# Performance work log

Measured on AMD Instinct MI355X. Metric: run time of the kernel, lower is better.

Reference implementation:

```python
import jax, jax.numpy as jnp
import numpy as np

N, E, ESM, H, OUT, L, NG = 20000, 640000, 1280, 128, 256, 3, 64
NV, EV = 4, 1  # node/edge vector channels
MSG_S, MSG_V = 2 * H + H, 2 * NV + EV   # 384, 9
UPD_S, UPD_V = 2 * H, 2 * NV            # 256, 8


def _safe_norm(v):
    # exact ||v|| with zero (not nan) gradient at v == 0
    n2 = jnp.sum(v * v, axis=-1)
    pos = n2 > 0
    return jnp.sqrt(jnp.where(pos, n2, 1.0)) * pos


def _normalize(x, eps=1e-12):
    n = _safe_norm(x)[..., None]
    return jnp.where(n > 0, x / jnp.maximum(n, eps), 0.0)


def _ln(x, g, b, eps=1e-5):
    m = x.mean(-1, keepdims=True)
    v = ((x - m) ** 2).mean(-1, keepdims=True)
    return (x - m) / jnp.sqrt(v + eps) * g + b


def _gvp(s, v, Wss, Wvs, Wsv, Wvv, g, b):
    # s: [M, Cs], v: [M, Cv, 3]
    vn = _safe_norm(v)                                        # [M, Cv]
    s_out = jax.nn.gelu(_ln(s @ Wss.T + vn @ Wvs.T, g, b), approximate=False)
    v_out = jnp.einsum('mic,oi->moc', v, Wvv)                 # [M, Cvo, 3]
    v_out = v_out * jax.nn.sigmoid(s @ Wsv.T)[:, :, None]     # gate from input s
    return s_out, v_out


def _compute_node_vectors(coords, cb):
    ca_cb = _normalize(cb - coords)
    ca_next = jnp.roll(coords, -1, axis=0)
    d = (ca_next - coords).at[-1].set(0.0)
    d = _normalize(d)
    normal = _normalize(jnp.cross(ca_cb, d))
    t = (ca_next - jnp.roll(coords, 1, axis=0)).at[0].set(0.0).at[-1].set(0.0)
    t = _normalize(t)
    return jnp.stack([ca_cb, d, normal, t], axis=1)           # [N, 4, 3]


def setup_inputs() -> dict:
    key = jax.random.key(0)
    ks = jax.random.split(key, 32)

    def w(k, shape):
        return (jax.random.normal(k, shape, jnp.float32) / np.sqrt(shape[-1])).astype(jnp.float32)

    inp = {
        'esm_features': jax.random.normal(ks[0], (N, ESM), jnp.float32),
        'geometric_features': jax.random.normal(ks[1], (N, 15), jnp.float32),
        'node_coords': jax.random.normal(ks[2], (N, 3), jnp.float32) * 10.0,
        'edge_index': jax.random.randint(ks[3], (2, E), 0, N, jnp.int32),
        'edge_attr': jax.random.normal(ks[4], (E, 16), jnp.float32),
        'batch_index': jnp.sort(jax.random.randint(ks[5], (N,), 0, NG, jnp.int32)),
        # projections
        'node_proj_W': w(ks[6], (H, ESM + 9)), 'node_proj_b': jnp.zeros((H,), jnp.float32),
        'edge_proj_W': w(ks[7], (H, 13)), 'edge_proj_b': jnp.zeros((H,), jnp.float32),
        # message GVP (stacked over L layers)
        'msg_Wss': w(ks[8], (L, H, MSG_S)), 'msg_Wvs': w(ks[9], (L, H, MSG_V)),
        'msg_Wsv': w(ks[10], (L, NV, MSG_S)), 'msg_Wvv': w(ks[11], (L, NV, MSG_V)),
        'msg_ln_g': jnp.ones((L, H), jnp.float32), 'msg_ln_b': jnp.zeros((L, H), jnp.float32),
        # update GVP
        'upd_Wss': w(ks[12], (L, H, UPD_S)), 'upd_Wvs': w(ks[13], (L, H, UPD_V)),
        'upd_Wsv': w(ks[14], (L, NV, UPD_S)), 'upd_Wvv': w(ks[15], (L, NV, UPD_V)),
        'upd_ln_g': jnp.ones((L, H), jnp.float32), 'upd_ln_b': jnp.zeros((L, H), jnp.float32),
        # heads
        'node_out_W': w(ks[16], (ESM, H)), 'node_out_b': jnp.zeros((ESM,), jnp.float32),
        'graph_out_W': w(ks[17], (OUT, H)), 'graph_out_b': jnp.zeros((OUT,), jnp.float32),
    }
    return inp


def reference(esm_features, geometric_features, node_coords, edge_index, edge_attr,
              batch_index, node_proj_W, node_proj_b, edge_proj_W, edge_proj_b,
              msg_Wss, msg_Wvs, msg_Wsv, msg_Wvv, msg_ln_g, msg_ln_b,
              upd_Wss, upd_Wvs, upd_Wsv, upd_Wvv, upd_ln_g, upd_ln_b,
              node_out_W, node_out_b, graph_out_W, graph_out_b):
    n = esm_features.shape[0]
    cb = geometric_features[:, 3:6]
    geo_scalar = geometric_features[:, 6:15]
    node_s = jnp.concatenate([esm_features, geo_scalar], -1) @ node_proj_W.T + node_proj_b
    node_v = _compute_node_vectors(node_coords, cb)
    edge_s = jnp.concatenate([edge_attr[:, 0:2], edge_attr[:, 5:]], -1) @ edge_proj_W.T + edge_proj_b
    edge_v = edge_attr[:, 2:5][:, None, :]                    # [E, 1, 3]
    src, dst = edge_index[0], edge_index[1]
    for l in range(msg_Wss.shape[0]):
        ms = jnp.concatenate([node_s[src], node_s[dst], edge_s], -1)   # [E, 3H]
        mv = jnp.concatenate([node_v[src], node_v[dst], edge_v], 1)    # [E, 9, 3]
        ms, mv = _gvp(ms, mv, msg_Wss[l], msg_Wvs[l], msg_Wsv[l], msg_Wvv[l],
                      msg_ln_g[l], msg_ln_b[l])
        ag_s = jnp.zeros((n, ms.shape[1]), ms.dtype).at[dst].add(ms)
        ag_v = jnp.zeros((n, mv.shape[1], 3), mv.dtype).at[dst].add(mv)
        us = jnp.concatenate([node_s, ag_s], -1)
        uv = jnp.concatenate([node_v, ag_v], 1)
        ns, nv = _gvp(us, uv, upd_Wss[l], upd_Wvs[l], upd_Wsv[l], upd_Wvv[l],
                      upd_ln_g[l], upd_ln_b[l])
        node_s = node_s + ns
        node_v = node_v + nv
    updated_nodes = node_s @ node_out_W.T + node_out_b
    gfeat = node_s @ graph_out_W.T + graph_out_b
    cnt = jax.ops.segment_sum(jnp.ones((n,), gfeat.dtype), batch_index, NG)
    graph_emb = jax.ops.segment_sum(gfeat, batch_index, NG) / jnp.maximum(cnt, 1.0)[:, None]
    return graph_emb, updated_nodes
```

## Files before the change

kernel.cpp:

```cpp
#include <hip/hip_runtime.h>
#include <math.h>

#define DEVI __device__ __forceinline__

namespace {

constexpr int NN = 20000;
constexpr int NE = 640000;

typedef __attribute__((ext_vector_type(8))) short s8v;
typedef __attribute__((ext_vector_type(4))) float f4v;

DEVI float gelu_f(float x){ return 0.5f*x*(1.0f+erff(x*0.70710678118654752440f)); }
DEVI float gelu_t(float x){
  float u = x*x;
  float z = x*(1.59576912f + 0.07135481f*u);
  return x / (1.f + __expf(-z));
}
DEVI float sigm(float x){ return 1.0f/(1.0f+expf(-x)); }
DEVI float sigm_f(float x){ return 1.0f/(1.0f+__expf(-x)); }
DEVI unsigned bf_rne(float f){ unsigned u=__float_as_uint(f); return (u + 0x7fffu + ((u>>16)&1u)) >> 16; }

struct F3{ float x,y,z; };
DEVI F3 sub3(F3 a, F3 b){ return F3{a.x-b.x, a.y-b.y, a.z-b.z}; }
DEVI F3 cross3(F3 a, F3 b){ return F3{a.y*b.z-a.z*b.y, a.z*b.x-a.x*b.z, a.x*b.y-a.y*b.x}; }
DEVI F3 snorm3(F3 v){
  float n2 = v.x*v.x+v.y*v.y+v.z*v.z;
  if(n2 > 0.f){ float inv = 1.0f/sqrtf(n2); return F3{v.x*inv, v.y*inv, v.z*inv}; }
  return F3{0.f,0.f,0.f};
}

__global__ void k_prep(const float* __restrict__ npW, const float* __restrict__ noW,
                       const float* __restrict__ goW,
                       const float* __restrict__ mWss, const float* __restrict__ mWvs,
                       const float* __restrict__ uWss, const float* __restrict__ uWvs,
                       unsigned short* __restrict__ npW_bf, float* __restrict__ Wt_no,
                       float* __restrict__ Wt_go,
                       float* __restrict__ Wt_mss, float* __restrict__ Wt_mvs,
                       float* __restrict__ Wt_uss, float* __restrict__ Wt_uvs){
  int b = blockIdx.x, t = threadIdx.x;
  if(b >= 1563){
    int idx = (b-1563)*256 + t;
    if(idx < 128*1408){
      int r = idx/1408, c = idx-r*1408;
      npW_bf[idx] = (c<1289) ? (unsigned short)bf_rne(npW[(size_t)r*1289+c]) : (unsigned short)0;
    }
    return;
  }
  const float* src; float* dst; int R,C,ld,base,elems;
  if(b<640){ src=noW; dst=Wt_no; R=1280;C=128;ld=128; base=0; elems=163840; }
  else if(b<768){ src=goW; dst=Wt_go; R=256;C=128;ld=128; base=640; elems=32768; }
  else {
    int bb=b-768; int l=bb/265; int r=bb-l*265;
    if(r<128){ src=mWss+(size_t)l*128*384; dst=Wt_mss+(size_t)l*256*128; R=128;C=256;ld=384; base=768+l*265; elems=32768; }
    else if(r<133){ src=mWvs+(size_t)l*128*9; dst=Wt_mvs+(size_t)l*9*128; R=128;C=9;ld=9; base=768+l*265+128; elems=1152; }
    else if(r<261){ src=uWss+(size_t)l*128*256; dst=Wt_uss+(size_t)l*256*128; R=128;C=256;ld=256; base=768+l*265+133; elems=32768; }
    else { src=uWvs+(size_t)l*128*8; dst=Wt_uvs+(size_t)l*8*128; R=128;C=8;ld=8; base=768+l*265+261; elems=1024; }
  }
  int idx=(b-base)*256+t;
  if(idx>=elems) return;
  int r=idx/C, c=idx%C;
  dst[c*R+r] = src[r*ld+c];
}

__global__ void k_conv(const float* __restrict__ esm, const float* __restrict__ geo,
                       unsigned short* __restrict__ esm_bf){
  int idx = blockIdx.x*256 + threadIdx.x;
  if(idx >= 20000*176) return;
  int r = idx/176, c = idx - r*176;
  int k = c*8;
  float v0,v1,v2,v3,v4,v5,v6,v7;
  if(k+8 <= 1280){
    const float4* p = reinterpret_cast<const float4*>(esm + (size_t)r*1280 + k);
    float4 x=p[0], y=p[1];
    v0=x.x;v1=x.y;v2=x.z;v3=x.w;v4=y.x;v5=y.y;v6=y.z;v7=y.w;
  } else {
    float vv[8];
#pragma unroll
    for(int j=0;j<8;j++){
      int kk=k+j;
      vv[j] = (kk<1280)? esm[(size_t)r*1280+kk] : ((kk<1289)? geo[r*15+6+(kk-1280)] : 0.f);
    }
    v0=vv[0];v1=vv[1];v2=vv[2];v3=vv[3];v4=vv[4];v5=vv[5];v6=vv[6];v7=vv[7];
  }
  uint4 w;
  w.x = bf_rne(v0) | (bf_rne(v1)<<16);
  w.y = bf_rne(v2) | (bf_rne(v3)<<16);
  w.z = bf_rne(v4) | (bf_rne(v5)<<16);
  w.w = bf_rne(v6) | (bf_rne(v7)<<16);
  reinterpret_cast<uint4*>(esm_bf)[idx] = w;
}

__global__ __launch_bounds__(256,4) void k_init(
    const unsigned short* __restrict__ esm_bf, const unsigned short* __restrict__ npW_bf,
    float* __restrict__ part){
  int t = threadIdx.x;
  int b = blockIdx.x;
  int ks = b & 3, nb = b >> 2;
  int wv = t>>6, lane = t&63;
  int row0 = nb*64 + wv*16;
  int arow = row0 + (lane&15);
  int arc = (arow < NN) ? arow : (NN-1);
  int kb = (lane>>4)*8;
  const unsigned short* ap = esm_bf + (size_t)arc*1408 + ks*352 + kb;
  const unsigned short* bp = npW_bf + (size_t)(lane&15)*1408 + ks*352 + kb;
  f4v acc[8];
#pragma unroll
  for(int i=0;i<8;i++) acc[i] = (f4v){0.f,0.f,0.f,0.f};
  for(int c=0;c<11;c++){
    s8v a = *reinterpret_cast<const s8v*>(ap + c*32);
#pragma unroll
    for(int nt=0;nt<8;nt++){
      s8v bb = *reinterpret_cast<const s8v*>(bp + (size_t)nt*16*1408 + c*32);
      acc[nt] = __builtin_amdgcn_mfma_f32_16x16x32_bf16(a, bb, acc[nt], 0,0,0);
    }
  }
  float* po = part + (size_t)ks*NN*128;
  int col = lane&15, r4 = (lane>>4)*4;
#pragma unroll
  for(int nt=0;nt<8;nt++){
    int o = nt*16+col;
#pragma unroll
    for(int r=0;r<4;r++){
      int row = row0 + r4 + r;
      if(row<NN) po[(size_t)row*128+o] = acc[nt][r];
    }
  }
}

__global__ void k_reduce(const float* __restrict__ part, const float* __restrict__ bias,
                         float* __restrict__ node_s){
  int idx = blockIdx.x*256 + threadIdx.x;
  int o = idx & 127;
  node_s[idx] = bias[o] + part[idx] + part[(size_t)NN*128+idx]
              + part[2*(size_t)NN*128+idx] + part[3*(size_t)NN*128+idx];
}

__global__ void k_nodevec(const float* __restrict__ coords, const float* __restrict__ geo,
                          float* __restrict__ node_v,
                          int* __restrict__ counts, int* __restrict__ cntg){
  int n = blockIdx.x*256 + threadIdx.x;
  if(n<64) cntg[n]=0;
  if(n>=NN) return;
  counts[n]=0;
  F3 c  {coords[n*3], coords[n*3+1], coords[n*3+2]};
  F3 cb {geo[n*15+3], geo[n*15+4], geo[n*15+5]};
  F3 cacb = snorm3(sub3(cb, c));
  F3 d{0.f,0.f,0.f};
  if(n < NN-1){
    F3 nx {coords[(n+1)*3], coords[(n+1)*3+1], coords[(n+1)*3+2]};
    d = snorm3(sub3(nx, c));
  }
  F3 nor = snorm3(cross3(cacb, d));
  F3 tv{0.f,0.f,0.f};
  if(n>0 && n<NN-1){
    F3 nx {coords[(n+1)*3], coords[(n+1)*3+1], coords[(n+1)*3+2]};
    F3 pv {coords[(n-1)*3], coords[(n-1)*3+1], coords[(n-1)*3+2]};
    tv = snorm3(sub3(nx, pv));
  }
  float* p = node_v + n*12;
  p[0]=cacb.x; p[1]=cacb.y; p[2]=cacb.z;
  p[3]=d.x;    p[4]=d.y;    p[5]=d.z;
  p[6]=nor.x;  p[7]=nor.y;  p[8]=nor.z;
  p[9]=tv.x;   p[10]=tv.y;  p[11]=tv.z;
}

__global__ void k_hist(const int* __restrict__ eidx, const int* __restrict__ batch,
                       int* __restrict__ counts, int* __restrict__ cntg){
  int i = blockIdx.x*256+threadIdx.x;
  if(i<NE) atomicAdd(&counts[eidx[NE+i]], 1);
  if(i<NN) atomicAdd(&cntg[batch[i]], 1);
}
__global__ void k_scan1(const int* __restrict__ counts, int* __restrict__ bsums){
  __shared__ int red[256];
  int b=blockIdx.x, t=threadIdx.x;
  int base=b*512;
  int v=0;
  for(int i=t;i<512;i+=256){ int g=base+i; if(g<NN) v+=counts[g]; }
  red[t]=v; __syncthreads();
  for(int s=128;s;s>>=1){ if(t<s) red[t]+=red[t+s]; __syncthreads(); }
  if(t==0) bsums[b]=red[0];
}
__global__ void k_scan23(const int* __restrict__ counts, const int* __restrict__ bsums,
                         int* __restrict__ offs, int* __restrict__ cursor){
  __shared__ int c_l[512];
  int b=blockIdx.x, t=threadIdx.x, base=b*512;
  for(int i=t;i<512;i+=256){ int g=base+i; c_l[i] = (g<NN)? counts[g]:0; }
  __syncthreads();
  if(t==0){
    int run=0;
    for(int i=0;i<b;i++) run += bsums[i];
    for(int i=0;i<512;i++){
      int g=base+i;
      if(g<NN){ offs[g]=run; cursor[g]=run; }
      run += c_l[i];
    }
    if(b==39) offs[NN]=run;
  }
}
__global__ void k_fill(const int* __restrict__ eidx, int* __restrict__ cursor,
                       const float* __restrict__ eattr,
                       int* __restrict__ srcp, float* __restrict__ ea_s){
  int e = blockIdx.x*256+threadIdx.x;
  if(e>=NE) return;
  int d = eidx[NE+e];
  int s = eidx[e];
  int pos = atomicAdd(&cursor[d], 1);
  srcp[pos] = s;
  const float4* src4 = reinterpret_cast<const float4*>(eattr + (size_t)e*16);
  float4* dst4 = reinterpret_cast<float4*>(ea_s + (size_t)pos*16);
  dst4[0]=src4[0]; dst4[1]=src4[1]; dst4[2]=src4[2]; dst4[3]=src4[3];
}

__global__ __launch_bounds__(256,4) void k_pre(
                      const float* __restrict__ node_s, const float* __restrict__ node_v,
                      const float* __restrict__ Wt_ss, const float* __restrict__ Wt_vs,
                      const float* __restrict__ Wsv, const float* __restrict__ Wvv,
                      float* __restrict__ P_a, float* __restrict__ P_b,
                      float* __restrict__ G_a, float* __restrict__ G_b,
                      float* __restrict__ V_a, float* __restrict__ V_b){
  __shared__ float s_l[16][128];
  __shared__ float nv_l[16][4];
  __shared__ float uv[16][12];
  int t = threadIdx.x;
  int n0 = blockIdx.x*16;
  for(int idx=t; idx<2048; idx+=256){
    int n = idx>>7, k = idx&127;
    s_l[n][k] = node_s[(size_t)(n0+n)*128 + k];
  }
  if(t<192){ int n=t/12, k=t%12; uv[n][k] = node_v[(n0+n)*12+k]; }
  __syncthreads();
  if(t<64){
    int n=t>>2, j=t&3;
    float x=uv[n][j*3], y=uv[n][j*3+1], z=uv[n][j*3+2];
    float n2=x*x+y*y+z*z;
    nv_l[n][j] = n2>0.f ? sqrtf(n2) : 0.f;
  }
  if(t<192){
    int n=t/12, k=t%12, c=k/3, x=k-c*3;
    float va=0.f, vb=0.f;
#pragma unroll
    for(int j=0;j<4;j++){
      float vv = uv[n][j*3+x];
      va += Wvv[c*9+j]*vv;
      vb += Wvv[c*9+4+j]*vv;
    }
    V_a[(n0+n)*12+k]=va; V_b[(n0+n)*12+k]=vb;
  }
  if(t<128){
    int n=t>>3, c=(t>>1)&3, hh=t&1;
    const float* w = Wsv + c*384 + hh*128;
    float g=0.f;
    for(int k=0;k<128;k+=4){
      float4 s4 = *reinterpret_cast<const float4*>(&s_l[n][k]);
      g = fmaf(s4.x,w[k],g); g = fmaf(s4.y,w[k+1],g);
      g = fmaf(s4.z,w[k+2],g); g = fmaf(s4.w,w[k+3],g);
    }
    (hh ? G_b : G_a)[(n0+n)*4+c] = g;
  }
  __syncthreads();
  int o = t&127, h = t>>7;
  float acc[16];
#pragma unroll
  for(int i=0;i<16;i++) acc[i]=0.f;
  const float* Wb = Wt_ss + h*128*128;
  for(int k=0;k<128;k+=4){
    float w0=Wb[(k+0)*128+o], w1=Wb[(k+1)*128+o], w2=Wb[(k+2)*128+o], w3=Wb[(k+3)*128+o];
#pragma unroll
    for(int n=0;n<16;n++){
      float4 s4 = *reinterpret_cast<const float4*>(&s_l[n][k]);
      acc[n] = fmaf(s4.x,w0,acc[n]); acc[n] = fmaf(s4.y,w1,acc[n]);
      acc[n] = fmaf(s4.z,w2,acc[n]); acc[n] = fmaf(s4.w,w3,acc[n]);
    }
  }
  const float* Wv = Wt_vs + h*4*128;
#pragma unroll
  for(int j=0;j<4;j++){
    float w = Wv[j*128+o];
#pragma unroll
    for(int n=0;n<16;n++) acc[n] += nv_l[n][j]*w;
  }
  float* P = h ? P_b : P_a;
  int oo = ((o&63)<<1) | (o>>6);
#pragma unroll
  for(int n=0;n<16;n++) P[(size_t)(n0+n)*128+oo] = acc[n];
}

__global__ void k_econst3(const float* __restrict__ mWss, const float* __restrict__ mWvs,
                          const float* __restrict__ mWsv, const float* __restrict__ mWvv,
                          const float* __restrict__ Wep, const float* __restrict__ epb,
                          float* __restrict__ econ){
  int l = blockIdx.x;
  const float* Wss = mWss + (size_t)l*128*384;
  const float* Wvs = mWvs + (size_t)l*128*9;
  const float* Wsv = mWsv + (size_t)l*4*384;
  const float* Wvv = mWvv + (size_t)l*4*9;
  float* ec = econ + (size_t)l*2048;
  int t=threadIdx.x;
  for(int idx=t; idx<13*128; idx+=256){
    int j=idx>>7, o=idx&127;
    float s=0.f;
    for(int k=0;k<128;k++) s += Wss[o*384+256+k]*Wep[k*13+j];
    ec[j*128+o]=s;
  }
  for(int o=t;o<128;o+=256){
    float s=0.f;
    for(int k=0;k<128;k++) s += Wss[o*384+256+k]*epb[k];
    ec[1664+o]=s;
    ec[1792+o]=Wvs[o*9+8];
  }
  if(t<52){ int c=t/13,j=t%13; float s=0.f; for(int k=0;k<128;k++) s+=Wsv[c*384+256+k]*Wep[k*13+j]; ec[1920+t]=s; }
  if(t<4){ float s=0.f; for(int k=0;k<128;k++) s+=Wsv[t*384+256+k]*epb[k]; ec[1972+t]=s; ec[1976+t]=Wvv[t*9+8]; }
}

__global__ __launch_bounds__(256,4) void k_edge(
    const float* __restrict__ ea_s, const float* __restrict__ ec,
    unsigned* __restrict__ preS2, float* __restrict__ preG){
  int t = threadIdx.x;
  int lane = t&63;
  int wid = blockIdx.x*4 + (t>>6);
  float mex[13], mey[13];
#pragma unroll
  for(int j=0;j<13;j++){ mex[j]=ec[j*128+lane]; mey[j]=ec[j*128+64+lane]; }
  float bx=ec[1664+lane], by=ec[1664+64+lane];
  float w8x=ec[1792+lane], w8y=ec[1792+64+lane];
  int cg = (lane<4)?lane:0;
  float grc[13];
#pragma unroll
  for(int j=0;j<13;j++) grc[j]=ec[1920+cg*13+j];
  float gb = ec[1972+cg];
  int e00 = wid*8;
#pragma unroll 2
  for(int i=0;i<8;i++){
    int e = e00+i;
    const float4* ea = reinterpret_cast<const float4*>(ea_s + (size_t)e*16);
    float4 A0=ea[0], A1=ea[1], A2=ea[2], A3=ea[3];
    float e0=A0.x,e1=A0.y,e2=A1.y,e3=A1.z,e4=A1.w,
          e5=A2.x,e6=A2.y,e7=A2.z,e8=A2.w,e9=A3.x,
          e10=A3.y,e11=A3.z,e12=A3.w;
    float evx=A0.z, evy=A0.w, evz=A1.x;
    float en2 = evx*evx+evy*evy+evz*evz;
    float evn = en2>0.f ? sqrtf(en2) : 0.f;
    float px = fmaf(evn,w8x,bx);
    float py = fmaf(evn,w8y,by);
    px=fmaf(mex[0],e0,px);   py=fmaf(mey[0],e0,py);
    px=fmaf(mex[1],e1,px);   py=fmaf(mey[1],e1,py);
    px=fmaf(mex[2],e2,px);   py=fmaf(mey[2],e2,py);
    px=fmaf(mex[3],e3,px);   py=fmaf(mey[3],e3,py);
    px=fmaf(mex[4],e4,px);   py=fmaf(mey[4],e4,py);
    px=fmaf(mex[5],e5,px);   py=fmaf(mey[5],e5,py);
    px=fmaf(mex[6],e6,px);   py=fmaf(mey[6],e6,py);
    px=fmaf(mex[7],e7,px);   py=fmaf(mey[7],e7,py);
    px=fmaf(mex[8],e8,px);   py=fmaf(mey[8],e8,py);
    px=fmaf(mex[9],e9,px);   py=fmaf(mey[9],e9,py);
    px=fmaf(mex[10],e10,px); py=fmaf(mey[10],e10,py);
    px=fmaf(mex[11],e11,px); py=fmaf(mey[11],e11,py);
    px=fmaf(mex[12],e12,px); py=fmaf(mey[12],e12,py);
    preS2[(size_t)e*64+lane] = bf_rne(px) | (bf_rne(py)<<16);
    if(lane<4){
      float g=gb;
      g=fmaf(grc[0],e0,g);  g=fmaf(grc[1],e1,g);  g=fmaf(grc[2],e2,g);
      g=fmaf(grc[3],e3,g);  g=fmaf(grc[4],e4,g);  g=fmaf(grc[5],e5,g);
      g=fmaf(grc[6],e6,g);  g=fmaf(grc[7],e7,g);  g=fmaf(grc[8],e8,g);
      g=fmaf(grc[9],e9,g);  g=fmaf(grc[10],e10,g); g=fmaf(grc[11],e11,g);
      g=fmaf(grc[12],e12,g);
      preG[(size_t)e*8+lane] = g;
    } else if(lane<7){
      float evv = (lane==4)?evx:((lane==5)?evy:evz);
      preG[(size_t)e*8+lane] = evv;
    }
  }
}

#define DECLST(P) unsigned P##w=0; float P##pax=0.f,P##pay=0.f,P##g8=0.f,P##ev=0.f,P##ga=0.f,P##va=0.f;
#define LOADST(P, IDX) do{ int _p=(IDX); \
  int _s = __builtin_amdgcn_readfirstlane(srcp[_p]); \
  P##w   = preS2[_p*64 + lane]; \
  float2 _pa = *reinterpret_cast<const float2*>(P_a + _s*128 + 2*lane); \
  P##pax = _pa.x; P##pay = _pa.y; \
  if(lane<12){ P##g8 = preG[_p*8+cv]; P##ev = preG[_p*8+4+xv]; \
               P##ga = G_a[_s*4+cv];  P##va = V_a[_s*12+lane]; } \
}while(0)
#define COMPUTE(P) do{ \
  float px = __uint_as_float(P##w<<16); \
  float py = __uint_as_float(P##w & 0xffff0000u); \
  float pre0 = px + P##pax + PBx; \
  float pre1 = py + P##pay + PBy; \
  float sm = pre0+pre1; \
  float sq = pre0*pre0 + pre1*pre1; \
  _Pragma("unroll") \
  for(int m=32;m;m>>=1){ sm += __shfl_xor(sm,m); sq += __shfl_xor(sq,m); } \
  float mean = sm*0.0078125f; \
  float var  = fmaf(sq,0.0078125f, -mean*mean); \
  float rstd = rsqrtf((var>0.f?var:0.f) + 1e-5f); \
  accx += gelu_t(fmaf((pre0-mean)*rstd, LGx, LBx)); \
  accy += gelu_t(fmaf((pre1-mean)*rstd, LGy, LBy)); \
  if(lane<12){ \
    float g = P##g8 + P##ga + gbn; \
    float gt = sigm_f(g); \
    avk = fmaf(fmaf(wvc, P##ev, P##va + vbk), gt, avk); \
  } \
}while(0)

__global__ __launch_bounds__(256,8) void k_msg(
                      const float* __restrict__ P_a, const float* __restrict__ P_b,
                      const float* __restrict__ G_a, const float* __restrict__ G_b,
                      const float* __restrict__ V_a, const float* __restrict__ V_b,
                      const unsigned* __restrict__ preS2, const float* __restrict__ preG,
                      const int* __restrict__ srcp, const int* __restrict__ offs,
                      const float* __restrict__ ec,
                      const float* __restrict__ lng, const float* __restrict__ lnb,
                      float* __restrict__ ag_s, float* __restrict__ ag_v){
  int t = threadIdx.x;
  int n = blockIdx.x*4 + (t>>6);
  int lane = t&63;
  float2 pb2 = *reinterpret_cast<const float2*>(P_b + n*128 + 2*lane);
  float PBx = pb2.x, PBy = pb2.y;
  float LGx = lng[lane], LGy = lng[64+lane];
  float LBx = lnb[lane], LBy = lnb[64+lane];
  int cv = lane/3, xv = lane - cv*3;
  float vbk=0.f, gbn=0.f, wvc=0.f;
  if(lane<12){
    vbk = V_b[n*12+lane];
    gbn = G_b[n*4+cv];
    wvc = ec[1976+cv];
  }
  float accx=0.f, accy=0.f, avk=0.f;
  int beg = offs[n], end = offs[n+1];
  DECLST(a_) DECLST(b_)
  int idx = beg;
  if(beg < end) LOADST(a_, beg);
  while(idx + 1 < end){
    LOADST(b_, idx+1);
    COMPUTE(a_);
    if(idx + 2 < end) LOADST(a_, idx+2);
    COMPUTE(b_);
    idx += 2;
  }
  if(idx < end) COMPUTE(a_);
  ag_s[n*128+lane]    = accx;
  ag_s[n*128+64+lane] = accy;
  if(lane<12) ag_v[n*12+lane] = avk;
}

__global__ __launch_bounds__(256,4) void k_update(
                         float* __restrict__ node_s, float* __restrict__ node_v,
                         const float* __restrict__ ag_s, const float* __restrict__ ag_v,
                         const float* __restrict__ Wt_ss, const float* __restrict__ Wt_vs,
                         const float* __restrict__ Wsv, const float* __restrict__ Wvv,
                         const float* __restrict__ lng, const float* __restrict__ lnb){
  __shared__ float us[16][260];
  __shared__ float pre[16][129];
  __shared__ float uv[16][24];
  __shared__ float uvn[16][8];
  __shared__ float stats[16][2];
  __shared__ float gate_l[16][4];
  int t = threadIdx.x;
  int n0 = blockIdx.x*16;
  for(int idx=t; idx<2048; idx+=256){
    int n = idx>>7, k = idx&127;
    us[n][k]     = node_s[(size_t)(n0+n)*128+k];
    us[n][128+k] = ag_s[(size_t)(n0+n)*128+k];
  }
  for(int idx=t; idx<384; idx+=256){
    int n = idx/24, k = idx%24;
    uv[n][k] = (k<12) ? node_v[(n0+n)*12+k] : ag_v[(n0+n)*12 + (k-12)];
  }
  __syncthreads();
  if(t<128){
    int n=t>>3, j=t&7;
    float x=uv[n][j*3], y=uv[n][j*3+1], z=uv[n][j*3+2];
    float n2=x*x+y*y+z*z;
    uvn[n][j] = n2>0.f ? sqrtf(n2) : 0.f;
  }
  __syncthreads();
  int o = t&127, h = t>>7;
  float acc[8];
#pragma unroll
  for(int i=0;i<8;i++) acc[i]=0.f;
  for(int k=0;k<256;k+=4){
    float w0=Wt_ss[(k+0)*128+o], w1=Wt_ss[(k+1)*128+o], w2=Wt_ss[(k+2)*128+o], w3=Wt_ss[(k+3)*128+o];
#pragma unroll
    for(int i=0;i<8;i++){
      float4 s4 = *reinterpret_cast<const float4*>(&us[h*8+i][k]);
      acc[i] = fmaf(s4.x,w0,acc[i]); acc[i] = fmaf(s4.y,w1,acc[i]);
      acc[i] = fmaf(s4.z,w2,acc[i]); acc[i] = fmaf(s4.w,w3,acc[i]);
    }
  }
#pragma unroll
  for(int j=0;j<8;j++){
    float w = Wt_vs[j*128+o];
#pragma unroll
    for(int i=0;i<8;i++) acc[i] += uvn[h*8+i][j]*w;
  }
#pragma unroll
  for(int i=0;i<8;i++) pre[h*8+i][o] = acc[i];
  __syncthreads();
  {
    int n = t>>4, p = t&15;
    float s=0.f;
#pragma unroll
    for(int q=0;q<8;q++) s += pre[n][p*8+q];
#pragma unroll
    for(int m=8;m;m>>=1) s += __shfl_xor(s,m);
    float mean = s*(1.f/128.f);
    float v=0.f;
#pragma unroll
    for(int q=0;q<8;q++){ float d=pre[n][p*8+q]-mean; v += d*d; }
#pragma unroll
    for(int m=8;m;m>>=1) v += __shfl_xor(v,m);
    if(p==0){ stats[n][0]=mean; stats[n][1]=rsqrtf(v*(1.f/128.f)+1e-5f); }
  }
  __syncthreads();
  {
    float LG = lng[o], LB = lnb[o];
#pragma unroll
    for(int i=0;i<8;i++){
      int n = h*8+i;
      float hh = (pre[n][o]-stats[n][0])*stats[n][1]*LG + LB;
      node_s[(size_t)(n0+n)*128+o] += gelu_f(hh);
    }
  }
  {
    int n = t>>4, c = t&3, p = (t>>2)&3;
    float g=0.f;
    int kb = p*64;
    for(int k=0;k<64;k+=4){
      float4 s4 = *reinterpret_cast<const float4*>(&us[n][kb+k]);
      g = fmaf(s4.x,Wsv[c*256+kb+k],g);   g = fmaf(s4.y,Wsv[c*256+kb+k+1],g);
      g = fmaf(s4.z,Wsv[c*256+kb+k+2],g); g = fmaf(s4.w,Wsv[c*256+kb+k+3],g);
    }
    g += __shfl_xor(g,4);
    g += __shfl_xor(g,8);
    if(p==0) gate_l[n][c] = sigm(g);
  }
  __syncthreads();
  if(t<192){
    int n = t/12, k = t%12, c = k/3, x = k-c*3;
    float s=0.f;
#pragma unroll
    for(int j=0;j<8;j++) s += Wvv[c*8+j]*uv[n][j*3+x];
    node_v[(n0+n)*12+k] += s*gate_l[n][c];
  }
}

__global__ __launch_bounds__(256,8) void k_out(
    const float* __restrict__ node_s, const float* __restrict__ Wt_no,
    const float* __restrict__ nob, float* __restrict__ out){
  __shared__ float s_l[32][132];
  int t = threadIdx.x;
  int n0 = blockIdx.x*32;
  int oc0 = blockIdx.y*256;
  {
    const float4* g = reinterpret_cast<const float4*>(node_s + (size_t)n0*128);
    for(int i=t;i<1024;i+=256){
      int n=i>>5, kq=i&31;
      *reinterpret_cast<float4*>(&s_l[n][kq*4]) = g[i];
    }
  }
  __syncthreads();
  int oq = t&63, ng = t>>6;
  int o = oc0 + oq*4;
  float4 acc[8];
#pragma unroll
  for(int i=0;i<8;i++) acc[i]=float4{0.f,0.f,0.f,0.f};
  for(int k=0;k<128;k+=4){
    float4 w0 = *reinterpret_cast<const float4*>(&Wt_no[(k+0)*1280+o]);
    float4 w1 = *reinterpret_cast<const float4*>(&Wt_no[(k+1)*1280+o]);
    float4 w2 = *reinterpret_cast<const float4*>(&Wt_no[(k+2)*1280+o]);
    float4 w3 = *reinterpret_cast<const float4*>(&Wt_no[(k+3)*1280+o]);
#pragma unroll
    for(int i=0;i<8;i++){
      float4 s = *reinterpret_cast<const float4*>(&s_l[ng*8+i][k]);
      acc[i].x=fmaf(s.x,w0.x,acc[i].x); acc[i].y=fmaf(s.x,w0.y,acc[i].y);
      acc[i].z=fmaf(s.x,w0.z,acc[i].z); acc[i].w=fmaf(s.x,w0.w,acc[i].w);
      acc[i].x=fmaf(s.y,w1.x,acc[i].x); acc[i].y=fmaf(s.y,w1.y,acc[i].y);
      acc[i].z=fmaf(s.y,w1.z,acc[i].z); acc[i].w=fmaf(s.y,w1.w,acc[i].w);
      acc[i].x=fmaf(s.z,w2.x,acc[i].x); acc[i].y=fmaf(s.z,w2.y,acc[i].y);
      acc[i].z=fmaf(s.z,w2.z,acc[i].z); acc[i].w=fmaf(s.z,w2.w,acc[i].w);
      acc[i].x=fmaf(s.w,w3.x,acc[i].x); acc[i].y=fmaf(s.w,w3.y,acc[i].y);
      acc[i].z=fmaf(s.w,w3.z,acc[i].z); acc[i].w=fmaf(s.w,w3.w,acc[i].w);
    }
  }
  float4 b4 = *reinterpret_cast<const float4*>(&nob[o]);
#pragma unroll
  for(int i=0;i<8;i++){
    int row = n0 + ng*8 + i;
    float4 r{acc[i].x+b4.x, acc[i].y+b4.y, acc[i].z+b4.z, acc[i].w+b4.w};
    *reinterpret_cast<float4*>(&out[16384 + (size_t)row*1280 + o]) = r;
  }
}

__global__ __launch_bounds__(256,4) void k_gfeat(
                        const float* __restrict__ node_s, const float* __restrict__ Wt,
                        const int* __restrict__ batch, float* __restrict__ gacc){
  __shared__ float s_l[16][128];
  __shared__ int b_l[16];
  int t=threadIdx.x, n0=blockIdx.x*16;
  for(int idx=t; idx<2048; idx+=256){ int n=idx>>7,k=idx&127; s_l[n][k]=node_s[(size_t)(n0+n)*128+k]; }
  if(t<16) b_l[t]=batch[n0+t];
  __syncthreads();
  int o=t;
  float acc[16];
#pragma unroll
  for(int i=0;i<16;i++) acc[i]=0.f;
  for(int k=0;k<128;k+=4){
    float w0=Wt[(k+0)*256+o], w1=Wt[(k+1)*256+o], w2=Wt[(k+2)*256+o], w3=Wt[(k+3)*256+o];
#pragma unroll
    for(int n=0;n<16;n++){
      float4 s4 = *reinterpret_cast<const float4*>(&s_l[n][k]);
      acc[n] = fmaf(s4.x,w0,acc[n]); acc[n] = fmaf(s4.y,w1,acc[n]);
      acc[n] = fmaf(s4.z,w2,acc[n]); acc[n] = fmaf(s4.w,w3,acc[n]);
    }
  }
  float run=0.f; int cur=b_l[0];
#pragma unroll
  for(int n=0;n<16;n++){
    int g=b_l[n];
    if(g!=cur){ atomicAdd(&gacc[cur*256+o], run); run=0.f; cur=g; }
    run += acc[n];
  }
  atomicAdd(&gacc[cur*256+o], run);
}

__global__ void k_gfin(const float* __restrict__ gacc, const int* __restrict__ cntg,
                       const float* __restrict__ gob, float* __restrict__ out){
  int g=blockIdx.x, o=threadIdx.x;
  int c=cntg[g];
  out[g*256+o] = (c>0) ? (gacc[g*256+o]/(float)c + gob[o]) : 0.f;
}

}

extern "C" void kernel_launch(void* const* d_in, const int* in_sizes, int n_in,
                              void* d_out, int out_size, void* d_ws, size_t ws_size,
                              hipStream_t stream){
  (void)in_sizes; (void)n_in; (void)out_size;
  const float* esm   = (const float*)d_in[0];
  const float* geo   = (const float*)d_in[1];
  const float* coords= (const float*)d_in[2];
  const int*   eidx  = (const int*)d_in[3];
  const float* eattr = (const float*)d_in[4];
  const int*   batch = (const int*)d_in[5];
  const float* npW   = (const float*)d_in[6];
  const float* npb   = (const float*)d_in[7];
  const float* epW   = (const float*)d_in[8];
  const float* epb   = (const float*)d_in[9];
  const float* mWss  = (const float*)d_in[10];
  const float* mWvs  = (const float*)d_in[11];
  const float* mWsv  = (const float*)d_in[12];
  const float* mWvv  = (const float*)d_in[13];
  const float* mlg   = (const float*)d_in[14];
  const float* mlb   = (const float*)d_in[15];
  const float* uWss  = (const float*)d_in[16];
  const float* uWvs  = (const float*)d_in[17];
  const float* uWsv  = (const float*)d_in[18];
  const float* uWvv  = (const float*)d_in[19];
  const float* ulg   = (const float*)d_in[20];
  const float* ulb   = (const float*)d_in[21];
  const float* noW   = (const float*)d_in[22];
  const float* nob   = (const float*)d_in[23];
  const float* goW   = (const float*)d_in[24];
  const float* gob   = (const float*)d_in[25];
  float* out = (float*)d_out;

  char* base = (char*)d_ws;
  size_t off = 0;
  auto ALLOC = [&](size_t bytes)->char*{
    char* p = base + off;
    off = (off + bytes + 255) & ~(size_t)255;
    return p;
  };
  float* node_s = (float*)ALLOC((size_t)NN*128*4);
  float* P_a    = (float*)ALLOC((size_t)NN*128*4);
  float* P_b    = (float*)ALLOC((size_t)NN*128*4);
  float* ag_s   = (float*)ALLOC((size_t)NN*128*4);
  float* node_v = (float*)ALLOC((size_t)NN*12*4);
  float* ag_v   = (float*)ALLOC((size_t)NN*12*4);
  float* V_a    = (float*)ALLOC((size_t)NN*12*4);
  float* V_b    = (float*)ALLOC((size_t)NN*12*4);
  float* G_a    = (float*)ALLOC((size_t)NN*4*4);
  float* G_b    = (float*)ALLOC((size_t)NN*4*4);
  unsigned short* npW_bf = (unsigned short*)ALLOC((size_t)128*1408*2);
  unsigned short* esm_bf = (unsigned short*)ALLOC((size_t)NN*1408*2);
  float* Wt_no  = (float*)ALLOC((size_t)128*1280*4);
  float* Wt_go  = (float*)ALLOC((size_t)128*256*4);
  float* Wt_mss = (float*)ALLOC((size_t)3*256*128*4);
  float* Wt_mvs = (float*)ALLOC((size_t)3*9*128*4);
  float* Wt_uss = (float*)ALLOC((size_t)3*256*128*4);
  float* Wt_uvs = (float*)ALLOC((size_t)3*8*128*4);
  float* econ   = (float*)ALLOC((size_t)3*2048*4);
  float* gacc   = (float*)ALLOC((size_t)64*256*4);
  int* counts = (int*)ALLOC((size_t)NN*4);
  int* offs   = (int*)ALLOC((size_t)(NN+1)*4);
  int* cursor = (int*)ALLOC((size_t)NN*4);
  int* bsums  = (int*)ALLOC((size_t)64*4);
  int* cntg   = (int*)ALLOC((size_t)64*4);
  int* srcp   = (int*)ALLOC((size_t)NE*4);
  float* ea_s = (float*)ALLOC((size_t)NE*16*4);
  unsigned* preS2 = (unsigned*)ALLOC((size_t)NE*64*4);
  float* preG     = (float*)ALLOC((size_t)NE*8*4);
  if(off > ws_size) return;
  float* part = (float*)preS2;

  hipMemsetAsync(gacc, 0, (size_t)64*256*4, stream);

  k_prep<<<2267,256,0,stream>>>(npW, noW, goW, mWss, mWvs, uWss, uWvs,
                                npW_bf, Wt_no, Wt_go, Wt_mss, Wt_mvs, Wt_uss, Wt_uvs);
  k_conv<<<13750,256,0,stream>>>(esm, geo, esm_bf);
  k_init<<<1252,256,0,stream>>>(esm_bf, npW_bf, part);
  k_reduce<<<10000,256,0,stream>>>(part, npb, node_s);
  k_nodevec<<<79,256,0,stream>>>(coords, geo, node_v, counts, cntg);
  k_hist<<<2500,256,0,stream>>>(eidx, batch, counts, cntg);
  k_scan1<<<40,256,0,stream>>>(counts, bsums);
  k_scan23<<<40,256,0,stream>>>(counts, bsums, offs, cursor);
  k_fill<<<2500,256,0,stream>>>(eidx, cursor, eattr, srcp, ea_s);
  k_econst3<<<3,256,0,stream>>>(mWss, mWvs, mWsv, mWvv, epW, epb, econ);

  for(int l=0;l<3;l++){
    k_pre<<<1250,256,0,stream>>>(node_s, node_v,
                                 Wt_mss + (size_t)l*256*128, Wt_mvs + (size_t)l*9*128,
                                 mWsv + (size_t)l*4*384, mWvv + (size_t)l*4*9,
                                 P_a, P_b, G_a, G_b, V_a, V_b);
    k_edge<<<20000,256,0,stream>>>(ea_s, econ + (size_t)l*2048, preS2, preG);
    k_msg<<<5000,256,0,stream>>>(P_a, P_b, G_a, G_b, V_a, V_b, preS2, preG, srcp, offs,
                                 econ + (size_t)l*2048, mlg + (size_t)l*128, mlb + (size_t)l*128,
                                 ag_s, ag_v);
    k_update<<<1250,256,0,stream>>>(node_s, node_v, ag_s, ag_v,
                                    Wt_uss + (size_t)l*256*128, Wt_uvs + (size_t)l*8*128,
                                    uWsv + (size_t)l*4*256, uWvv + (size_t)l*4*8,
                                    ulg + (size_t)l*128, ulb + (size_t)l*128);
  }
  k_out<<<dim3(625,5),256,0,stream>>>(node_s, Wt_no, nob, out);
  k_gfeat<<<1250,256,0,stream>>>(node_s, Wt_go, batch, gacc);
  k_gfin<<<64,256,0,stream>>>(gacc, cntg, gob, out);
}
```

Baseline: 1.550 ms.

## Fuse edge projection into message kernel and precompute edge gates once

The per-layer k_edge pass is removed. It wrote a bf16-packed 128-wide edge projection for every edge, which k_msg then read back. k_msg now keeps the 13x128 edge-projection weights in registers and recomputes the projection from a compact 16-float per-edge record (ea_m, built in k_fill and including the precomputed vector norm). The small gate terms for all three layers are computed once up front in a new k_edge3 kernel. This swaps a large per-layer write and read of edge intermediates for extra FMAs and more registers in k_msg, whose launch bound drops from 8 to 4 waves and may reduce occupancy.

```diff
diff --git a/kernel.cpp b/kernel.cpp
--- a/kernel.cpp
+++ b/kernel.cpp
@@ -200,7 +200,8 @@
 }
 __global__ void k_fill(const int* __restrict__ eidx, int* __restrict__ cursor,
                        const float* __restrict__ eattr,
-                       int* __restrict__ srcp, float* __restrict__ ea_s){
+                       int* __restrict__ srcp, float* __restrict__ ea_s,
+                       float* __restrict__ ea_m){
   int e = blockIdx.x*256+threadIdx.x;
   if(e>=NE) return;
   int d = eidx[NE+e];
@@ -208,8 +209,17 @@
   int pos = atomicAdd(&cursor[d], 1);
   srcp[pos] = s;
   const float4* src4 = reinterpret_cast<const float4*>(eattr + (size_t)e*16);
+  float4 A0=src4[0], A1=src4[1], A2=src4[2], A3=src4[3];
   float4* dst4 = reinterpret_cast<float4*>(ea_s + (size_t)pos*16);
-  dst4[0]=src4[0]; dst4[1]=src4[1]; dst4[2]=src4[2]; dst4[3]=src4[3];
+  dst4[0]=A0; dst4[1]=A1; dst4[2]=A2; dst4[3]=A3;
+  float evx=A0.z, evy=A0.w, evz=A1.x;
+  float en2 = evx*evx+evy*evy+evz*evz;
+  float evn = en2>0.f ? sqrtf(en2) : 0.f;
+  float4* m4 = reinterpret_cast<float4*>(ea_m + (size_t)pos*16);
+  m4[0] = float4{A0.x, A0.y, A1.y, A1.z};
+  m4[1] = float4{A1.w, A2.x, A2.y, A2.z};
+  m4[2] = float4{A2.w, A3.x, A3.y, A3.z};
+  m4[3] = float4{A3.w, evn, 0.f, 0.f};
 }
 
 __global__ __launch_bounds__(256,4) void k_pre(
@@ -313,88 +323,70 @@
   if(t<4){ float s=0.f; for(int k=0;k<128;k++) s+=Wsv[t*384+256+k]*epb[k]; ec[1972+t]=s; ec[1976+t]=Wvv[t*9+8]; }
 }
 
-__global__ __launch_bounds__(256,4) void k_edge(
-    const float* __restrict__ ea_s, const float* __restrict__ ec,
-    unsigned* __restrict__ preS2, float* __restrict__ preG){
-  int t = threadIdx.x;
-  int lane = t&63;
-  int wid = blockIdx.x*4 + (t>>6);
-  float mex[13], mey[13];
-#pragma unroll
-  for(int j=0;j<13;j++){ mex[j]=ec[j*128+lane]; mey[j]=ec[j*128+64+lane]; }
-  float bx=ec[1664+lane], by=ec[1664+64+lane];
-  float w8x=ec[1792+lane], w8y=ec[1792+64+lane];
-  int cg = (lane<4)?lane:0;
-  float grc[13];
-#pragma unroll
-  for(int j=0;j<13;j++) grc[j]=ec[1920+cg*13+j];
-  float gb = ec[1972+cg];
-  int e00 = wid*8;
-#pragma unroll 2
-  for(int i=0;i<8;i++){
-    int e = e00+i;
-    const float4* ea = reinterpret_cast<const float4*>(ea_s + (size_t)e*16);
-    float4 A0=ea[0], A1=ea[1], A2=ea[2], A3=ea[3];
-    float e0=A0.x,e1=A0.y,e2=A1.y,e3=A1.z,e4=A1.w,
-          e5=A2.x,e6=A2.y,e7=A2.z,e8=A2.w,e9=A3.x,
-          e10=A3.y,e11=A3.z,e12=A3.w;
-    float evx=A0.z, evy=A0.w, evz=A1.x;
-    float en2 = evx*evx+evy*evy+evz*evz;
-    float evn = en2>0.f ? sqrtf(en2) : 0.f;
-    float px = fmaf(evn,w8x,bx);
-    float py = fmaf(evn,w8y,by);
-    px=fmaf(mex[0],e0,px);   py=fmaf(mey[0],e0,py);
-    px=fmaf(mex[1],e1,px);   py=fmaf(mey[1],e1,py);
-    px=fmaf(mex[2],e2,px);   py=fmaf(mey[2],e2,py);
-    px=fmaf(mex[3],e3,px);   py=fmaf(mey[3],e3,py);
-    px=fmaf(mex[4],e4,px);   py=fmaf(mey[4],e4,py);
-    px=fmaf(mex[5],e5,px);   py=fmaf(mey[5],e5,py);
-    px=fmaf(mex[6],e6,px);   py=fmaf(mey[6],e6,py);
-    px=fmaf(mex[7],e7,px);   py=fmaf(mey[7],e7,py);
-    px=fmaf(mex[8],e8,px);   py=fmaf(mey[8],e8,py);
-    px=fmaf(mex[9],e9,px);   py=fmaf(mey[9],e9,py);
-    px=fmaf(mex[10],e10,px); py=fmaf(mey[10],e10,py);
-    px=fmaf(mex[11],e11,px); py=fmaf(mey[11],e11,py);
-    px=fmaf(mex[12],e12,px); py=fmaf(mey[12],e12,py);
-    preS2[(size_t)e*64+lane] = bf_rne(px) | (bf_rne(py)<<16);
-    if(lane<4){
-      float g=gb;
-      g=fmaf(grc[0],e0,g);  g=fmaf(grc[1],e1,g);  g=fmaf(grc[2],e2,g);
-      g=fmaf(grc[3],e3,g);  g=fmaf(grc[4],e4,g);  g=fmaf(grc[5],e5,g);
-      g=fmaf(grc[6],e6,g);  g=fmaf(grc[7],e7,g);  g=fmaf(grc[8],e8,g);
-      g=fmaf(grc[9],e9,g);  g=fmaf(grc[10],e10,g); g=fmaf(grc[11],e11,g);
-      g=fmaf(grc[12],e12,g);
-      preG[(size_t)e*8+lane] = g;
-    } else if(lane<7){
-      float evv = (lane==4)?evx:((lane==5)?evy:evz);
-      preG[(size_t)e*8+lane] = evv;
-    }
-  }
-}
-
-#define DECLST(P) unsigned P##w=0; float P##pax=0.f,P##pay=0.f,P##g8=0.f,P##ev=0.f,P##ga=0.f,P##va=0.f;
-#define LOADST(P, IDX) do{ int _p=(IDX); \
-  int _s = __builtin_amdgcn_readfirstlane(srcp[_p]); \
-  P##w   = preS2[_p*64 + lane]; \
+__global__ __launch_bounds__(256,4) void k_edge3(
+    const float* __restrict__ ea_s, const float* __restrict__ econ,
+    float* __restrict__ preG3){
+  int e = blockIdx.x*256+threadIdx.x;
+  if(e>=NE) return;
+  const float4* ea = reinterpret_cast<const float4*>(ea_s + (size_t)e*16);
+  float4 A0=ea[0], A1=ea[1], A2=ea[2], A3=ea[3];
+  float ein[13] = {A0.x, A0.y, A1.y, A1.z, A1.w, A2.x, A2.y, A2.z, A2.w,
+                   A3.x, A3.y, A3.z, A3.w};
+  float evx=A0.z, evy=A0.w, evz=A1.x;
+#pragma unroll
+  for(int l=0;l<3;l++){
+    const float* ec = econ + l*2048;
+    float4 g4;
+    float* gp = reinterpret_cast<float*>(&g4);
+#pragma unroll
+    for(int c=0;c<4;c++){
+      float g = ec[1972+c];
+#pragma unroll
+      for(int j=0;j<13;j++) g = fmaf(ec[1920+c*13+j], ein[j], g);
+      gp[c] = g;
+    }
+    float4* po = reinterpret_cast<float4*>(preG3 + (size_t)l*NE*8 + (size_t)e*8);
+    po[0] = g4;
+    po[1] = float4{evx, evy, evz, 0.f};
+  }
+}
+
+#define DECLST(P) float4 P##A0{},P##A1{},P##A2{},P##A3{}; \
+                  float P##pax=0.f,P##pay=0.f,P##g8=0.f,P##ev=0.f,P##ga=0.f,P##va=0.f;
+#define LOADST(P, IDX) do{ int _p=(IDX); int _s=srcp[_p]; \
+  const float4* _em = reinterpret_cast<const float4*>(ea_m + (size_t)_p*16); \
+  P##A0=_em[0]; P##A1=_em[1]; P##A2=_em[2]; P##A3=_em[3]; \
   float2 _pa = *reinterpret_cast<const float2*>(P_a + _s*128 + 2*lane); \
   P##pax = _pa.x; P##pay = _pa.y; \
   if(lane<12){ P##g8 = preG[_p*8+cv]; P##ev = preG[_p*8+4+xv]; \
                P##ga = G_a[_s*4+cv];  P##va = V_a[_s*12+lane]; } \
 }while(0)
 #define COMPUTE(P) do{ \
-  float px = __uint_as_float(P##w<<16); \
-  float py = __uint_as_float(P##w & 0xffff0000u); \
-  float pre0 = px + P##pax + PBx; \
-  float pre1 = py + P##pay + PBy; \
-  float sm = pre0+pre1; \
-  float sq = pre0*pre0 + pre1*pre1; \
+  float evn = P##A3.y; \
+  float px = fmaf(evn, W8x, P##pax + PBx); \
+  float py = fmaf(evn, W8y, P##pay + PBy); \
+  px=fmaf(me2x[0],P##A0.x,px);  py=fmaf(me2y[0],P##A0.x,py); \
+  px=fmaf(me2x[1],P##A0.y,px);  py=fmaf(me2y[1],P##A0.y,py); \
+  px=fmaf(me2x[2],P##A0.z,px);  py=fmaf(me2y[2],P##A0.z,py); \
+  px=fmaf(me2x[3],P##A0.w,px);  py=fmaf(me2y[3],P##A0.w,py); \
+  px=fmaf(me2x[4],P##A1.x,px);  py=fmaf(me2y[4],P##A1.x,py); \
+  px=fmaf(me2x[5],P##A1.y,px);  py=fmaf(me2y[5],P##A1.y,py); \
+  px=fmaf(me2x[6],P##A1.z,px);  py=fmaf(me2y[6],P##A1.z,py); \
+  px=fmaf(me2x[7],P##A1.w,px);  py=fmaf(me2y[7],P##A1.w,py); \
+  px=fmaf(me2x[8],P##A2.x,px);  py=fmaf(me2y[8],P##A2.x,py); \
+  px=fmaf(me2x[9],P##A2.y,px);  py=fmaf(me2y[9],P##A2.y,py); \
+  px=fmaf(me2x[10],P##A2.z,px); py=fmaf(me2y[10],P##A2.z,py); \
+  px=fmaf(me2x[11],P##A2.w,px); py=fmaf(me2y[11],P##A2.w,py); \
+  px=fmaf(me2x[12],P##A3.x,px); py=fmaf(me2y[12],P##A3.x,py); \
+  float sm = px+py; \
+  float sq = px*px + py*py; \
   _Pragma("unroll") \
   for(int m=32;m;m>>=1){ sm += __shfl_xor(sm,m); sq += __shfl_xor(sq,m); } \
   float mean = sm*0.0078125f; \
   float var  = fmaf(sq,0.0078125f, -mean*mean); \
   float rstd = rsqrtf((var>0.f?var:0.f) + 1e-5f); \
-  accx += gelu_t(fmaf((pre0-mean)*rstd, LGx, LBx)); \
-  accy += gelu_t(fmaf((pre1-mean)*rstd, LGy, LBy)); \
+  accx += gelu_t(fmaf((px-mean)*rstd, LGx, LBx)); \
+  accy += gelu_t(fmaf((py-mean)*rstd, LGy, LBy)); \
   if(lane<12){ \
     float g = P##g8 + P##ga + gbn; \
     float gt = sigm_f(g); \
@@ -402,11 +394,11 @@
   } \
 }while(0)
 
-__global__ __launch_bounds__(256,8) void k_msg(
+__global__ __launch_bounds__(256,4) void k_msg(
                       const float* __restrict__ P_a, const float* __restrict__ P_b,
                       const float* __restrict__ G_a, const float* __restrict__ G_b,
                       const float* __restrict__ V_a, const float* __restrict__ V_b,
-                      const unsigned* __restrict__ preS2, const float* __restrict__ preG,
+                      const float* __restrict__ ea_m, const float* __restrict__ preG,
                       const int* __restrict__ srcp, const int* __restrict__ offs,
                       const float* __restrict__ ec,
                       const float* __restrict__ lng, const float* __restrict__ lnb,
@@ -414,8 +406,13 @@
   int t = threadIdx.x;
   int n = blockIdx.x*4 + (t>>6);
   int lane = t&63;
+  float me2x[13], me2y[13];
+#pragma unroll
+  for(int j=0;j<13;j++){ me2x[j]=ec[j*128+lane]; me2y[j]=ec[j*128+64+lane]; }
   float2 pb2 = *reinterpret_cast<const float2*>(P_b + n*128 + 2*lane);
-  float PBx = pb2.x, PBy = pb2.y;
+  float PBx = pb2.x + ec[1664+lane];
+  float PBy = pb2.y + ec[1664+64+lane];
+  float W8x = ec[1792+lane], W8y = ec[1792+64+lane];
   float LGx = lng[lane], LGy = lng[64+lane];
   float LBx = lnb[lane], LBy = lnb[64+lane];
   int cv = lane/3, xv = lane - cv*3;
@@ -698,10 +695,11 @@
   int* cntg   = (int*)ALLOC((size_t)64*4);
   int* srcp   = (int*)ALLOC((size_t)NE*4);
   float* ea_s = (float*)ALLOC((size_t)NE*16*4);
-  unsigned* preS2 = (unsigned*)ALLOC((size_t)NE*64*4);
-  float* preG     = (float*)ALLOC((size_t)NE*8*4);
+  float* big  = (float*)ALLOC((size_t)NE*16*4 + (size_t)3*NE*8*4);
   if(off > ws_size) return;
-  float* part = (float*)preS2;
+  float* part  = big;
+  float* ea_m  = big;
+  float* preG3 = big + (size_t)NE*16;
 
   hipMemsetAsync(gacc, 0, (size_t)64*256*4, stream);
 
@@ -714,16 +712,17 @@
   k_hist<<<2500,256,0,stream>>>(eidx, batch, counts, cntg);
   k_scan1<<<40,256,0,stream>>>(counts, bsums);
   k_scan23<<<40,256,0,stream>>>(counts, bsums, offs, cursor);
-  k_fill<<<2500,256,0,stream>>>(eidx, cursor, eattr, srcp, ea_s);
+  k_fill<<<2500,256,0,stream>>>(eidx, cursor, eattr, srcp, ea_s, ea_m);
   k_econst3<<<3,256,0,stream>>>(mWss, mWvs, mWsv, mWvv, epW, epb, econ);
+  k_edge3<<<2500,256,0,stream>>>(ea_s, econ, preG3);
 
   for(int l=0;l<3;l++){
     k_pre<<<1250,256,0,stream>>>(node_s, node_v,
                                  Wt_mss + (size_t)l*256*128, Wt_mvs + (size_t)l*9*128,
                                  mWsv + (size_t)l*4*384, mWvv + (size_t)l*4*9,
                                  P_a, P_b, G_a, G_b, V_a, V_b);
-    k_edge<<<20000,256,0,stream>>>(ea_s, econ + (size_t)l*2048, preS2, preG);
-    k_msg<<<5000,256,0,stream>>>(P_a, P_b, G_a, G_b, V_a, V_b, preS2, preG, srcp, offs,
+    k_msg<<<5000,256,0,stream>>>(P_a, P_b, G_a, G_b, V_a, V_b, ea_m,
+                                 preG3 + (size_t)l*NE*8, srcp, offs,
                                  econ + (size_t)l*2048, mlg + (size_t)l*128, mlb + (size_t)l*128,
                                  ag_s, ag_v);
     k_update<<<1250,256,0,stream>>>(node_s, node_v, ag_s, ag_v,
```

Result: slower. 1.787 ms (+15.3%).
